# Optimization experiments

Measured on AMD Instinct MI355X. Metric: run time of the kernel, lower is better.

Reference implementation:

```python
import jax, jax.numpy as jnp
import numpy as np
import math

E, H, FFN, NQ = 1024, 16, 4096, 8
B, T = 2, 2048
EPS = 1e-5

def layernorm(x, g, b):
    mu = jnp.mean(x, axis=-1, keepdims=True)
    var = jnp.mean(jnp.square(x - mu), axis=-1, keepdims=True)
    return (x - mu) * jax.lax.rsqrt(var + EPS) * g + b

def setup_inputs() -> dict:
    key = jax.random.key(0)
    ks = jax.random.split(key, 8)
    x = jax.random.normal(ks[0], (B, T, E), dtype=jnp.float32)
    mask = jnp.ones((B, T, T), dtype=bool)
    # constant quantum measurement output: PauliZ expectations of a fixed
    # RandomLayer circuit applied to |0..0> (independent of the input tokens)
    q_out = jax.random.uniform(ks[1], (NQ,), minval=-1.0, maxval=1.0, dtype=jnp.float32)
    s1 = 1.0 / math.sqrt(NQ)
    w1 = jax.random.uniform(ks[2], (NQ, FFN), minval=-s1, maxval=s1, dtype=jnp.float32)
    b1 = jnp.zeros((FFN,), dtype=jnp.float32)
    s2 = 1.0 / math.sqrt(FFN)
    w2 = jax.random.uniform(ks[3], (FFN, E), minval=-s2, maxval=s2, dtype=jnp.float32)
    b2 = jnp.zeros((E,), dtype=jnp.float32)
    g1 = jnp.ones((E,), dtype=jnp.float32); be1 = jnp.zeros((E,), dtype=jnp.float32)
    g2 = jnp.ones((E,), dtype=jnp.float32); be2 = jnp.zeros((E,), dtype=jnp.float32)
    return dict(x=x, mask=mask, q_out=q_out, w1=w1, b1=b1, w2=w2, b2=b2,
                g1=g1, be1=be1, g2=g2, be2=be2)

def reference(x, mask, q_out, w1, b1, w2, b2, g1, be1, g2, be2):
    b, t, e = x.shape
    d_k = e // H
    # q = k = v = head-split x (module has no QKV projections)
    q = x.reshape(b, t, H, d_k).transpose(0, 2, 1, 3)  # [B,H,T,d_k]
    scores = jnp.einsum('bhqd,bhkd->bhqk', q, q) / math.sqrt(d_k)
    scores = jnp.where(mask[:, None, :, :], scores, -1e9)
    attn = jax.nn.softmax(scores, axis=-1)
    out = jnp.einsum('bhqk,bhkd->bhqd', attn, q)
    attn_out = out.transpose(0, 2, 1, 3).reshape(b, t, e)
    x1 = layernorm(x + attn_out, g1, be1)
    # quantum FFN: constant measurement vector broadcast over all tokens
    h = jnp.broadcast_to(q_out, (b, t, NQ))
    h = jnp.dot(h, w1) + b1
    ffn_out = jnp.dot(jax.nn.relu(h), w2) + b2
    return layernorm(x1 + ffn_out, g2, be2)
```

## Files before the change

### kernel.cpp

```cpp
#include <hip/hip_runtime.h>

#define E_   1024
#define H_   16
#define DK_  64
#define FFN_ 4096
#define NQ_  8
#define B_   2
#define T_   2048
#define QBLK 128
#define KVBLK 64
#define NT_  (T_ / KVBLK)

#define NPART 256
#define ROWS_PER_PART (FFN_ / NPART)

typedef __attribute__((ext_vector_type(8))) __bf16 bf16x8;
typedef __attribute__((ext_vector_type(4))) float f32x4;
typedef __attribute__((ext_vector_type(16))) float f32x16;

__device__ __forceinline__ __bf16 tobf(float f) { return (__bf16)f; }

__device__ __forceinline__ unsigned pk2(float a, float b) {
  union { __bf16 h; unsigned short u; } ua, ub;
  ua.h = (__bf16)a; ub.h = (__bf16)b;
  return (unsigned)ua.u | ((unsigned)ub.u << 16);
}

__global__ __launch_bounds__(256)
void cvt_kernel(const float* __restrict__ x, __bf16* __restrict__ xbf,
                __bf16* __restrict__ xbfT) {
  __shared__ __bf16 tile[64][66];
  const int tid = threadIdx.x;
  const int bid = blockIdx.x;
  const int h  = bid & 15;
  const int tt = (bid >> 4) & 31;
  const int b  = bid >> 9;
  const float* src = x + ((size_t)(b * T_ + tt * 64)) * E_ + h * 64;

#pragma unroll
  for (int u = 0; u < 2; ++u) {
    const int idx = tid + 256 * u;
    const int r = idx >> 3;
    const int c = (idx & 7) * 8;
    float4 f0 = *reinterpret_cast<const float4*>(src + (size_t)r * E_ + c);
    float4 f1 = *reinterpret_cast<const float4*>(src + (size_t)r * E_ + c + 4);
    bf16x8 v;
    v[0] = tobf(f0.x); v[1] = tobf(f0.y); v[2] = tobf(f0.z); v[3] = tobf(f0.w);
    v[4] = tobf(f1.x); v[5] = tobf(f1.y); v[6] = tobf(f1.z); v[7] = tobf(f1.w);
    *reinterpret_cast<bf16x8*>(
        &xbf[((size_t)(b * T_ + tt * 64 + r)) * E_ + h * 64 + c]) = v;
#pragma unroll
    for (int j = 0; j < 8; ++j) tile[r][c + j] = v[j];
  }
  __syncthreads();
#pragma unroll
  for (int u = 0; u < 2; ++u) {
    const int idx = tid + 256 * u;
    const int d  = idx >> 3;
    const int tc = (idx & 7) * 8;
    bf16x8 v;
#pragma unroll
    for (int j = 0; j < 8; ++j) v[j] = tile[tc + j][d];
    *reinterpret_cast<bf16x8*>(
        &xbfT[((size_t)((b * H_ + h) * DK_ + d)) * T_ + tt * 64 + tc]) = v;
  }
}

__global__ __launch_bounds__(256)
void ffn_part_kernel(const float* __restrict__ q_out, const float* __restrict__ w1,
                     const float* __restrict__ b1, const float* __restrict__ w2,
                     float* __restrict__ part) {
  __shared__ float h[ROWS_PER_PART];
  const int tid = threadIdx.x;
  const int p = blockIdx.x;
  const int f0 = p * ROWS_PER_PART;
  if (tid < ROWS_PER_PART) {
    const int f = f0 + tid;
    float a = b1[f];
#pragma unroll
    for (int n = 0; n < NQ_; ++n) a += q_out[n] * w1[n * FFN_ + f];
    h[tid] = fmaxf(a, 0.f);
  }
  __syncthreads();
  float4 acc = {0.f, 0.f, 0.f, 0.f};
#pragma unroll
  for (int j = 0; j < ROWS_PER_PART; ++j) {
    const float hf = h[j];
    float4 w = reinterpret_cast<const float4*>(w2 + (size_t)(f0 + j) * E_)[tid];
    acc.x += hf * w.x; acc.y += hf * w.y; acc.z += hf * w.z; acc.w += hf * w.w;
  }
  reinterpret_cast<float4*>(part + (size_t)p * E_)[tid] = acc;
}

__global__ __launch_bounds__(256)
void ffn_reduce_kernel(const float* __restrict__ part, const float* __restrict__ b2,
                       float* __restrict__ ffn_c) {
  const int e = blockIdx.x * 256 + threadIdx.x;
  float a = b2[e];
  for (int r = 0; r < NPART; ++r) a += part[(size_t)r * E_ + e];
  ffn_c[e] = a;
}

#define PV_STEP(KS, DARR, OARR)                                                \
  do {                                                                         \
    const int mA = 2 * ((KS) & 1), mB = mA + 1;                                \
    union { unsigned u[4]; bf16x8 v; } pa;                                     \
    pa.u[0] = hi ? OARR[mB][0] : DARR[mA][0];                                  \
    pa.u[1] = hi ? OARR[mB][1] : DARR[mA][1];                                  \
    pa.u[2] = hi ? DARR[mB][0] : OARR[mA][0];                                  \
    pa.u[3] = hi ? DARR[mB][1] : OARR[mA][1];                                  \
    bf16x8 vb0 = *reinterpret_cast<const bf16x8*>(                             \
        Vtc + rowA + (((32 * (KS) + 16 * hi) ^ rxA)));                         \
    bf16x8 vb1 = *reinterpret_cast<const bf16x8*>(                             \
        Vtc + rowB + (((32 * (KS) + 16 * hi) ^ rxB)));                         \
    acc0 = __builtin_amdgcn_mfma_f32_32x32x16_bf16(pa.v, vb0, acc0, 0, 0, 0);  \
    acc1 = __builtin_amdgcn_mfma_f32_32x32x16_bf16(pa.v, vb1, acc1, 0, 0, 0);  \
  } while (0)

__global__ __launch_bounds__(256)
void attn_kernel(const __bf16* __restrict__ xbf, const __bf16* __restrict__ xbfT,
                 float* __restrict__ out) {
  __shared__ __bf16 Kt[2][KVBLK][DK_ + 8];
  __shared__ __bf16 VtF[2][DK_ * KVBLK];

  const int tid  = threadIdx.x;
  const int wave = tid >> 6;
  const int lane = tid & 63;
  const int l32  = lane & 31;
  const int hi   = lane >> 5;

  const int bh = blockIdx.y;
  const int b  = bh >> 4;
  const int h  = bh & 15;
  const int qbase = blockIdx.x * QBLK;
  const __bf16* xb = xbf + (size_t)b * T_ * E_ + h * DK_;

  bf16x8 qb[4];
  {
    const __bf16 sc = (__bf16)0.125f;
    const __bf16* qrow = xb + (size_t)(qbase + wave * 32 + l32) * E_;
#pragma unroll
    for (int ks = 0; ks < 4; ++ks) {
      bf16x8 v = *reinterpret_cast<const bf16x8*>(qrow + 16 * ks + 8 * hi);
#pragma unroll
      for (int j = 0; j < 8; ++j) v[j] *= sc;
      qb[ks] = v;
    }
  }

  f32x16 acc0, acc1;
#pragma unroll
  for (int j = 0; j < 16; ++j) { acc0[j] = 0.f; acc1[j] = 0.f; }
  float lg = 0.f;

  const int rotA = (l32 & 7) ^ ((l32 >> 3) & 7);
  const int rotB = (l32 & 7) ^ ((4 + (l32 >> 3)) & 7);
  const int rowA = l32 * 128, rxA = rotA << 4;
  const int rowB = (32 + l32) * 128, rxB = rotB << 4;

  const int kp  = tid >> 3;
  const int ds0 = (tid & 7) * 8;
  const __bf16* kbase = xb + (size_t)(2 * kp) * E_ + ds0;
  const int dv = tid >> 3;
  const int kv = (tid & 7) * 8;
  const __bf16* vbase = xbfT + ((size_t)(bh * DK_ + dv)) * T_ + kv;
  const int srotA = (dv & 7) ^ ((dv >> 3) & 7);
  const int dvB = dv + 32;
  const int srotB = (dvB & 7) ^ ((dvB >> 3) & 7);
  const int vbyteA = dv * 128 + ((kv * 2) ^ (srotA << 4));
  const int vbyteB = dvB * 128 + ((kv * 2) ^ (srotB << 4));

  {
    uint4 k0 = *reinterpret_cast<const uint4*>(kbase);
    uint4 k1 = *reinterpret_cast<const uint4*>(kbase + E_);
    uint4 v0 = *reinterpret_cast<const uint4*>(vbase);
    uint4 v1 = *reinterpret_cast<const uint4*>(vbase + (size_t)32 * T_);
    *reinterpret_cast<uint4*>(&Kt[0][2 * kp][ds0])     = k0;
    *reinterpret_cast<uint4*>(&Kt[0][2 * kp + 1][ds0]) = k1;
    char* vb = reinterpret_cast<char*>(&VtF[0][0]);
    *reinterpret_cast<uint4*>(vb + vbyteA) = v0;
    *reinterpret_cast<uint4*>(vb + vbyteB) = v1;
  }
  __syncthreads();

  for (int t = 0; t < NT_; ++t) {
    const int cur = t & 1;
    const __bf16* Ktc = &Kt[cur][0][0];
    const char*   Vtc = reinterpret_cast<const char*>(&VtF[cur][0]);

    uint4 nk0, nk1, nv0, nv1;
    const bool have_next = (t + 1 < NT_);
    if (have_next) {
      const __bf16* nk = kbase + (size_t)(t + 1) * KVBLK * E_;
      const __bf16* nv = vbase + (size_t)(t + 1) * KVBLK;
      nk0 = *reinterpret_cast<const uint4*>(nk);
      nk1 = *reinterpret_cast<const uint4*>(nk + E_);
      nv0 = *reinterpret_cast<const uint4*>(nv);
      nv1 = *reinterpret_cast<const uint4*>(nv + (size_t)32 * T_);
    }

    f32x16 s0, s1;
#pragma unroll
    for (int j = 0; j < 16; ++j) { s0[j] = 0.f; s1[j] = 0.f; }
    __builtin_amdgcn_s_setprio(1);
#pragma unroll
    for (int ks = 0; ks < 4; ++ks) {
      bf16x8 ka0 = *reinterpret_cast<const bf16x8*>(
          Ktc + (size_t)l32 * (DK_ + 8) + 16 * ks + 8 * hi);
      bf16x8 ka1 = *reinterpret_cast<const bf16x8*>(
          Ktc + (size_t)(32 + l32) * (DK_ + 8) + 16 * ks + 8 * hi);
      s0 = __builtin_amdgcn_mfma_f32_32x32x16_bf16(ka0, qb[ks], s0, 0, 0, 0);
      s1 = __builtin_amdgcn_mfma_f32_32x32x16_bf16(ka1, qb[ks], s1, 0, 0, 0);
    }
    __builtin_amdgcn_s_setprio(0);

    unsigned dA_[4][2], dB_[4][2], oA_[4][2], oB_[4][2];
#pragma unroll
    for (int m = 0; m < 4; ++m) {
      float a0 = __expf(s0[4 * m + 0]), a1 = __expf(s0[4 * m + 1]);
      float a2 = __expf(s0[4 * m + 2]), a3 = __expf(s0[4 * m + 3]);
      lg += (a0 + a1) + (a2 + a3);
      dA_[m][0] = pk2(a0, a1); dA_[m][1] = pk2(a2, a3);
      float b0 = __expf(s1[4 * m + 0]), b1 = __expf(s1[4 * m + 1]);
      float b2 = __expf(s1[4 * m + 2]), b3 = __expf(s1[4 * m + 3]);
      lg += (b0 + b1) + (b2 + b3);
      dB_[m][0] = pk2(b0, b1); dB_[m][1] = pk2(b2, b3);
    }
#pragma unroll
    for (int m = 0; m < 4; ++m) {
      oA_[m][0] = (unsigned)__shfl_xor((int)dA_[m][0], 32);
      oA_[m][1] = (unsigned)__shfl_xor((int)dA_[m][1], 32);
      oB_[m][0] = (unsigned)__shfl_xor((int)dB_[m][0], 32);
      oB_[m][1] = (unsigned)__shfl_xor((int)dB_[m][1], 32);
    }

    __builtin_amdgcn_s_setprio(1);
    PV_STEP(0, dA_, oA_);
    PV_STEP(1, dA_, oA_);
    PV_STEP(2, dB_, oB_);
    PV_STEP(3, dB_, oB_);
    __builtin_amdgcn_s_setprio(0);

    if (have_next) {
      const int nxt = cur ^ 1;
      *reinterpret_cast<uint4*>(&Kt[nxt][2 * kp][ds0])     = nk0;
      *reinterpret_cast<uint4*>(&Kt[nxt][2 * kp + 1][ds0]) = nk1;
      char* vb = reinterpret_cast<char*>(&VtF[nxt][0]);
      *reinterpret_cast<uint4*>(vb + vbyteA) = nv0;
      *reinterpret_cast<uint4*>(vb + vbyteB) = nv1;
    }
    __syncthreads();
  }

  lg += __shfl_xor(lg, 32);
#pragma unroll
  for (int r = 0; r < 16; ++r) {
    const int qw = (r & 3) + 8 * (r >> 2) + 4 * hi;
    const float inv = 1.f / __shfl(lg, qw);
    const size_t q = (size_t)b * T_ + qbase + wave * 32 + qw;
    out[q * E_ + h * 64 + l32]      = acc0[r] * inv;
    out[q * E_ + h * 64 + 32 + l32] = acc1[r] * inv;
  }
}

__device__ __forceinline__ float block_sum(float v, float* redrow, int lane, int wave) {
#pragma unroll
  for (int off = 1; off < 64; off <<= 1) v += __shfl_xor(v, off);
  if (lane == 0) redrow[wave] = v;
  __syncthreads();
  return redrow[0] + redrow[1] + redrow[2] + redrow[3];
}

__global__ __launch_bounds__(256)
void ln_kernel(const float* __restrict__ x, const float* __restrict__ ffn_c,
               const float* __restrict__ g1, const float* __restrict__ be1,
               const float* __restrict__ g2, const float* __restrict__ be2,
               float* io) {
  __shared__ float red[4][4];
  const int row = blockIdx.x;
  const int tid = threadIdx.x;
  const int lane = tid & 63, wave = tid >> 6;
  const float* xr = x + (size_t)row * E_;
  float* ior = io + (size_t)row * E_;

  float4 xv = reinterpret_cast<const float4*>(xr)[tid];
  float4 av = reinterpret_cast<const float4*>(ior)[tid];
  float v[4] = {xv.x + av.x, xv.y + av.y, xv.z + av.z, xv.w + av.w};

  float mu1 = block_sum(v[0] + v[1] + v[2] + v[3], red[0], lane, wave) * (1.f / E_);
  float q1 = 0.f;
#pragma unroll
  for (int j = 0; j < 4; ++j) { float d = v[j] - mu1; q1 += d * d; }
  float var1 = block_sum(q1, red[1], lane, wave) * (1.f / E_);
  float rs1 = rsqrtf(var1 + 1e-5f);

  const int e0 = tid * 4;
  float y[4];
#pragma unroll
  for (int j = 0; j < 4; ++j)
    y[j] = (v[j] - mu1) * rs1 * g1[e0 + j] + be1[e0 + j] + ffn_c[e0 + j];

  float mu2 = block_sum(y[0] + y[1] + y[2] + y[3], red[2], lane, wave) * (1.f / E_);
  float q2 = 0.f;
#pragma unroll
  for (int j = 0; j < 4; ++j) { float d = y[j] - mu2; q2 += d * d; }
  float var2 = block_sum(q2, red[3], lane, wave) * (1.f / E_);
  float rs2 = rsqrtf(var2 + 1e-5f);

  float4 o;
  o.x = (y[0] - mu2) * rs2 * g2[e0 + 0] + be2[e0 + 0];
  o.y = (y[1] - mu2) * rs2 * g2[e0 + 1] + be2[e0 + 1];
  o.z = (y[2] - mu2) * rs2 * g2[e0 + 2] + be2[e0 + 2];
  o.w = (y[3] - mu2) * rs2 * g2[e0 + 3] + be2[e0 + 3];
  reinterpret_cast<float4*>(ior)[tid] = o;
}

extern "C" void kernel_launch(void* const* d_in, const int* in_sizes, int n_in,
                              void* d_out, int out_size, void* d_ws, size_t ws_size,
                              hipStream_t stream) {
  (void)in_sizes; (void)n_in; (void)out_size; (void)ws_size;
  const float* x     = (const float*)d_in[0];
  const float* q_out = (const float*)d_in[2];
  const float* w1    = (const float*)d_in[3];
  const float* b1    = (const float*)d_in[4];
  const float* w2    = (const float*)d_in[5];
  const float* b2    = (const float*)d_in[6];
  const float* g1    = (const float*)d_in[7];
  const float* be1   = (const float*)d_in[8];
  const float* g2    = (const float*)d_in[9];
  const float* be2   = (const float*)d_in[10];
  float* out   = (float*)d_out;

  float* ffn_c = (float*)d_ws;
  float* part  = ffn_c + E_;
  __bf16* xbf  = (__bf16*)(part + (size_t)NPART * E_);
  __bf16* xbfT = xbf + (size_t)B_ * T_ * E_;

  cvt_kernel<<<B_ * (T_ / 64) * H_, 256, 0, stream>>>(x, xbf, xbfT);
  ffn_part_kernel<<<NPART, 256, 0, stream>>>(q_out, w1, b1, w2, part);
  ffn_reduce_kernel<<<E_ / 256, 256, 0, stream>>>(part, b2, ffn_c);
  dim3 ag(T_ / QBLK, B_ * H_);
  attn_kernel<<<ag, 256, 0, stream>>>(xbf, xbfT, out);
  ln_kernel<<<B_ * T_, 256, 0, stream>>>(x, ffn_c, g1, be1, g2, be2, out);
}
```

Baseline: 97.10 us.

## Merge prep kernels and streamline attention softmax with exp2 and permlane swap

The bf16 conversion/transpose kernel and the FFN partial kernel become one launch whose block index picks the work, which removes one kernel launch and lets the two jobs overlap. In the attention loop, log2(e) is folded into the query scale so exp2 replaces expf. The cross-half shuffles plus per-lane selects that built the PV operand are replaced by v_permlane32_swap, and bf16 packing now uses a vector conversion. The risks are slightly different bf16 rounding of the pre-scaled query and reliance on an inline-asm instruction specific to the target architecture.

```diff
diff --git a/kernel.cpp b/kernel.cpp
--- a/kernel.cpp
+++ b/kernel.cpp
@@ -13,83 +13,85 @@
 
 #define NPART 256
 #define ROWS_PER_PART (FFN_ / NPART)
+#define CVT_BLOCKS (B_ * (T_ / 64) * H_)
 
 typedef __attribute__((ext_vector_type(8))) __bf16 bf16x8;
+typedef __attribute__((ext_vector_type(2))) __bf16 bf16x2;
+typedef __attribute__((ext_vector_type(2))) float f32x2;
 typedef __attribute__((ext_vector_type(4))) float f32x4;
 typedef __attribute__((ext_vector_type(16))) float f32x16;
 
 __device__ __forceinline__ __bf16 tobf(float f) { return (__bf16)f; }
 
 __device__ __forceinline__ unsigned pk2(float a, float b) {
-  union { __bf16 h; unsigned short u; } ua, ub;
-  ua.h = (__bf16)a; ub.h = (__bf16)b;
-  return (unsigned)ua.u | ((unsigned)ub.u << 16);
+  f32x2 f; f[0] = a; f[1] = b;
+  bf16x2 h = __builtin_convertvector(f, bf16x2);
+  union { bf16x2 h; unsigned u; } u; u.h = h;
+  return u.u;
 }
 
 __global__ __launch_bounds__(256)
-void cvt_kernel(const float* __restrict__ x, __bf16* __restrict__ xbf,
-                __bf16* __restrict__ xbfT) {
-  __shared__ __bf16 tile[64][66];
+void prep_kernel(const float* __restrict__ x, __bf16* __restrict__ xbf,
+                 __bf16* __restrict__ xbfT,
+                 const float* __restrict__ q_out, const float* __restrict__ w1,
+                 const float* __restrict__ b1, const float* __restrict__ w2,
+                 float* __restrict__ part) {
   const int tid = threadIdx.x;
-  const int bid = blockIdx.x;
-  const int h  = bid & 15;
-  const int tt = (bid >> 4) & 31;
-  const int b  = bid >> 9;
-  const float* src = x + ((size_t)(b * T_ + tt * 64)) * E_ + h * 64;
-
-#pragma unroll
-  for (int u = 0; u < 2; ++u) {
-    const int idx = tid + 256 * u;
-    const int r = idx >> 3;
-    const int c = (idx & 7) * 8;
-    float4 f0 = *reinterpret_cast<const float4*>(src + (size_t)r * E_ + c);
-    float4 f1 = *reinterpret_cast<const float4*>(src + (size_t)r * E_ + c + 4);
-    bf16x8 v;
-    v[0] = tobf(f0.x); v[1] = tobf(f0.y); v[2] = tobf(f0.z); v[3] = tobf(f0.w);
-    v[4] = tobf(f1.x); v[5] = tobf(f1.y); v[6] = tobf(f1.z); v[7] = tobf(f1.w);
-    *reinterpret_cast<bf16x8*>(
-        &xbf[((size_t)(b * T_ + tt * 64 + r)) * E_ + h * 64 + c]) = v;
-#pragma unroll
-    for (int j = 0; j < 8; ++j) tile[r][c + j] = v[j];
-  }
-  __syncthreads();
-#pragma unroll
-  for (int u = 0; u < 2; ++u) {
-    const int idx = tid + 256 * u;
-    const int d  = idx >> 3;
-    const int tc = (idx & 7) * 8;
-    bf16x8 v;
-#pragma unroll
-    for (int j = 0; j < 8; ++j) v[j] = tile[tc + j][d];
-    *reinterpret_cast<bf16x8*>(
-        &xbfT[((size_t)((b * H_ + h) * DK_ + d)) * T_ + tt * 64 + tc]) = v;
-  }
-}
-
-__global__ __launch_bounds__(256)
-void ffn_part_kernel(const float* __restrict__ q_out, const float* __restrict__ w1,
-                     const float* __restrict__ b1, const float* __restrict__ w2,
-                     float* __restrict__ part) {
-  __shared__ float h[ROWS_PER_PART];
-  const int tid = threadIdx.x;
-  const int p = blockIdx.x;
-  const int f0 = p * ROWS_PER_PART;
-  if (tid < ROWS_PER_PART) {
-    const int f = f0 + tid;
-    float a = b1[f];
-#pragma unroll
-    for (int n = 0; n < NQ_; ++n) a += q_out[n] * w1[n * FFN_ + f];
-    h[tid] = fmaxf(a, 0.f);
-  }
-  __syncthreads();
-  float4 acc = {0.f, 0.f, 0.f, 0.f};
-#pragma unroll
-  for (int j = 0; j < ROWS_PER_PART; ++j) {
-    const float hf = h[j];
-    float4 w = reinterpret_cast<const float4*>(w2 + (size_t)(f0 + j) * E_)[tid];
-    acc.x += hf * w.x; acc.y += hf * w.y; acc.z += hf * w.z; acc.w += hf * w.w;
-  }
-  reinterpret_cast<float4*>(part + (size_t)p * E_)[tid] = acc;
+  if (blockIdx.x < CVT_BLOCKS) {
+    __shared__ __bf16 tile[64][66];
+    const int bid = blockIdx.x;
+    const int h  = bid & 15;
+    const int tt = (bid >> 4) & 31;
+    const int b  = bid >> 9;
+    const float* src = x + ((size_t)(b * T_ + tt * 64)) * E_ + h * 64;
+#pragma unroll
+    for (int u = 0; u < 2; ++u) {
+      const int idx = tid + 256 * u;
+      const int r = idx >> 3;
+      const int c = (idx & 7) * 8;
+      float4 f0 = *reinterpret_cast<const float4*>(src + (size_t)r * E_ + c);
+      float4 f1 = *reinterpret_cast<const float4*>(src + (size_t)r * E_ + c + 4);
+      bf16x8 v;
+      v[0] = tobf(f0.x); v[1] = tobf(f0.y); v[2] = tobf(f0.z); v[3] = tobf(f0.w);
+      v[4] = tobf(f1.x); v[5] = tobf(f1.y); v[6] = tobf(f1.z); v[7] = tobf(f1.w);
+      *reinterpret_cast<bf16x8*>(
+          &xbf[((size_t)(b * T_ + tt * 64 + r)) * E_ + h * 64 + c]) = v;
+#pragma unroll
+      for (int j = 0; j < 8; ++j) tile[r][c + j] = v[j];
+    }
+    __syncthreads();
+#pragma unroll
+    for (int u = 0; u < 2; ++u) {
+      const int idx = tid + 256 * u;
+      const int d  = idx >> 3;
+      const int tc = (idx & 7) * 8;
+      bf16x8 v;
+#pragma unroll
+      for (int j = 0; j < 8; ++j) v[j] = tile[tc + j][d];
+      *reinterpret_cast<bf16x8*>(
+          &xbfT[((size_t)((b * H_ + h) * DK_ + d)) * T_ + tt * 64 + tc]) = v;
+    }
+  } else {
+    __shared__ float hbuf[ROWS_PER_PART];
+    const int p = blockIdx.x - CVT_BLOCKS;
+    const int f0 = p * ROWS_PER_PART;
+    if (tid < ROWS_PER_PART) {
+      const int f = f0 + tid;
+      float a = b1[f];
+#pragma unroll
+      for (int n = 0; n < NQ_; ++n) a += q_out[n] * w1[n * FFN_ + f];
+      hbuf[tid] = fmaxf(a, 0.f);
+    }
+    __syncthreads();
+    float4 acc = {0.f, 0.f, 0.f, 0.f};
+#pragma unroll
+    for (int j = 0; j < ROWS_PER_PART; ++j) {
+      const float hf = hbuf[j];
+      float4 w = reinterpret_cast<const float4*>(w2 + (size_t)(f0 + j) * E_)[tid];
+      acc.x += hf * w.x; acc.y += hf * w.y; acc.z += hf * w.z; acc.w += hf * w.w;
+    }
+    reinterpret_cast<float4*>(part + (size_t)p * E_)[tid] = acc;
+  }
 }
 
 __global__ __launch_bounds__(256)
@@ -101,20 +103,45 @@
   ffn_c[e] = a;
 }
 
-#define PV_STEP(KS, DARR, OARR)                                                \
+#define SM16(S, P)                                                             \
   do {                                                                         \
-    const int mA = 2 * ((KS) & 1), mB = mA + 1;                                \
+    _Pragma("unroll")                                                          \
+    for (int m = 0; m < 4; ++m) {                                              \
+      float e0 = __builtin_exp2f((S)[4 * m + 0]);                              \
+      float e1 = __builtin_exp2f((S)[4 * m + 1]);                              \
+      float e2 = __builtin_exp2f((S)[4 * m + 2]);                              \
+      float e3 = __builtin_exp2f((S)[4 * m + 3]);                              \
+      lg += (e0 + e1) + (e2 + e3);                                             \
+      (P)[m][0] = pk2(e0, e1); (P)[m][1] = pk2(e2, e3);                        \
+    }                                                                          \
+  } while (0)
+
+#define SWP(a, b) asm volatile("v_permlane32_swap_b32 %0, %1" : "+v"(a), "+v"(b))
+#define SW4(P)                                                                 \
+  do {                                                                         \
+    SWP((P)[0][0], (P)[1][0]); SWP((P)[0][1], (P)[1][1]);                      \
+    SWP((P)[2][0], (P)[3][0]); SWP((P)[2][1], (P)[3][1]);                      \
+  } while (0)
+
+#define PVQ(P, KSG)                                                            \
+  do {                                                                         \
     union { unsigned u[4]; bf16x8 v; } pa;                                     \
-    pa.u[0] = hi ? OARR[mB][0] : DARR[mA][0];                                  \
-    pa.u[1] = hi ? OARR[mB][1] : DARR[mA][1];                                  \
-    pa.u[2] = hi ? DARR[mB][0] : OARR[mA][0];                                  \
-    pa.u[3] = hi ? DARR[mB][1] : OARR[mA][1];                                  \
+    pa.u[0] = (P)[0][0]; pa.u[1] = (P)[0][1];                                  \
+    pa.u[2] = (P)[1][0]; pa.u[3] = (P)[1][1];                                  \
     bf16x8 vb0 = *reinterpret_cast<const bf16x8*>(                             \
-        Vtc + rowA + (((32 * (KS) + 16 * hi) ^ rxA)));                         \
+        Vtc + rowA + ((32 * (KSG) + 16 * hi) ^ rxA));                          \
     bf16x8 vb1 = *reinterpret_cast<const bf16x8*>(                             \
-        Vtc + rowB + (((32 * (KS) + 16 * hi) ^ rxB)));                         \
+        Vtc + rowB + ((32 * (KSG) + 16 * hi) ^ rxB));                          \
     acc0 = __builtin_amdgcn_mfma_f32_32x32x16_bf16(pa.v, vb0, acc0, 0, 0, 0);  \
     acc1 = __builtin_amdgcn_mfma_f32_32x32x16_bf16(pa.v, vb1, acc1, 0, 0, 0);  \
+    pa.u[0] = (P)[2][0]; pa.u[1] = (P)[2][1];                                  \
+    pa.u[2] = (P)[3][0]; pa.u[3] = (P)[3][1];                                  \
+    bf16x8 vc0 = *reinterpret_cast<const bf16x8*>(                             \
+        Vtc + rowA + ((32 * ((KSG) + 1) + 16 * hi) ^ rxA));                    \
+    bf16x8 vc1 = *reinterpret_cast<const bf16x8*>(                             \
+        Vtc + rowB + ((32 * ((KSG) + 1) + 16 * hi) ^ rxB));                    \
+    acc0 = __builtin_amdgcn_mfma_f32_32x32x16_bf16(pa.v, vc0, acc0, 0, 0, 0);  \
+    acc1 = __builtin_amdgcn_mfma_f32_32x32x16_bf16(pa.v, vc1, acc1, 0, 0, 0);  \
   } while (0)
 
 __global__ __launch_bounds__(256)
@@ -137,13 +164,13 @@
 
   bf16x8 qb[4];
   {
-    const __bf16 sc = (__bf16)0.125f;
+    const float sc = 0.125f * 1.44269504088896f;
     const __bf16* qrow = xb + (size_t)(qbase + wave * 32 + l32) * E_;
 #pragma unroll
     for (int ks = 0; ks < 4; ++ks) {
       bf16x8 v = *reinterpret_cast<const bf16x8*>(qrow + 16 * ks + 8 * hi);
 #pragma unroll
-      for (int j = 0; j < 8; ++j) v[j] *= sc;
+      for (int j = 0; j < 8; ++j) v[j] = tobf((float)v[j] * sc);
       qb[ks] = v;
     }
   }
@@ -153,10 +180,11 @@
   for (int j = 0; j < 16; ++j) { acc0[j] = 0.f; acc1[j] = 0.f; }
   float lg = 0.f;
 
-  const int rotA = (l32 & 7) ^ ((l32 >> 3) & 7);
-  const int rotB = (l32 & 7) ^ ((4 + (l32 >> 3)) & 7);
-  const int rowA = l32 * 128, rxA = rotA << 4;
-  const int rowB = (32 + l32) * 128, rxB = rotB << 4;
+  const int rowA = l32 * 128;
+  const int rxA  = ((l32 & 7) ^ ((l32 >> 3) & 7)) << 4;
+  const int d2   = 32 + l32;
+  const int rowB = d2 * 128;
+  const int rxB  = ((d2 & 7) ^ ((d2 >> 3) & 7)) << 4;
 
   const int kp  = tid >> 3;
   const int ds0 = (tid & 7) * 8;
@@ -164,11 +192,11 @@
   const int dv = tid >> 3;
   const int kv = (tid & 7) * 8;
   const __bf16* vbase = xbfT + ((size_t)(bh * DK_ + dv)) * T_ + kv;
-  const int srotA = (dv & 7) ^ ((dv >> 3) & 7);
-  const int dvB = dv + 32;
-  const int srotB = (dvB & 7) ^ ((dvB >> 3) & 7);
-  const int vbyteA = dv * 128 + ((kv * 2) ^ (srotA << 4));
-  const int vbyteB = dvB * 128 + ((kv * 2) ^ (srotB << 4));
+  const int srA = ((dv & 7) ^ ((dv >> 3) & 7)) << 4;
+  const int dv2 = dv + 32;
+  const int srB = ((dv2 & 7) ^ ((dv2 >> 3) & 7)) << 4;
+  const int vbyteA = dv * 128 + ((kv * 2) ^ srA);
+  const int vbyteB = dv2 * 128 + ((kv * 2) ^ srB);
 
   {
     uint4 k0 = *reinterpret_cast<const uint4*>(kbase);
@@ -214,31 +242,15 @@
     }
     __builtin_amdgcn_s_setprio(0);
 
-    unsigned dA_[4][2], dB_[4][2], oA_[4][2], oB_[4][2];
-#pragma unroll
-    for (int m = 0; m < 4; ++m) {
-      float a0 = __expf(s0[4 * m + 0]), a1 = __expf(s0[4 * m + 1]);
-      float a2 = __expf(s0[4 * m + 2]), a3 = __expf(s0[4 * m + 3]);
-      lg += (a0 + a1) + (a2 + a3);
-      dA_[m][0] = pk2(a0, a1); dA_[m][1] = pk2(a2, a3);
-      float b0 = __expf(s1[4 * m + 0]), b1 = __expf(s1[4 * m + 1]);
-      float b2 = __expf(s1[4 * m + 2]), b3 = __expf(s1[4 * m + 3]);
-      lg += (b0 + b1) + (b2 + b3);
-      dB_[m][0] = pk2(b0, b1); dB_[m][1] = pk2(b2, b3);
-    }
-#pragma unroll
-    for (int m = 0; m < 4; ++m) {
-      oA_[m][0] = (unsigned)__shfl_xor((int)dA_[m][0], 32);
-      oA_[m][1] = (unsigned)__shfl_xor((int)dA_[m][1], 32);
-      oB_[m][0] = (unsigned)__shfl_xor((int)dB_[m][0], 32);
-      oB_[m][1] = (unsigned)__shfl_xor((int)dB_[m][1], 32);
-    }
+    unsigned dA_[4][2], dB_[4][2];
+    SM16(s0, dA_);
+    SM16(s1, dB_);
+    SW4(dA_);
+    SW4(dB_);
 
     __builtin_amdgcn_s_setprio(1);
-    PV_STEP(0, dA_, oA_);
-    PV_STEP(1, dA_, oA_);
-    PV_STEP(2, dB_, oB_);
-    PV_STEP(3, dB_, oB_);
+    PVQ(dA_, 0);
+    PVQ(dB_, 2);
     __builtin_amdgcn_s_setprio(0);
 
     if (have_next) {
@@ -336,8 +348,8 @@
   __bf16* xbf  = (__bf16*)(part + (size_t)NPART * E_);
   __bf16* xbfT = xbf + (size_t)B_ * T_ * E_;
 
-  cvt_kernel<<<B_ * (T_ / 64) * H_, 256, 0, stream>>>(x, xbf, xbfT);
-  ffn_part_kernel<<<NPART, 256, 0, stream>>>(q_out, w1, b1, w2, part);
+  prep_kernel<<<CVT_BLOCKS + NPART, 256, 0, stream>>>(x, xbf, xbfT, q_out, w1,
+                                                      b1, w2, part);
   ffn_reduce_kernel<<<E_ / 256, 256, 0, stream>>>(part, b2, ffn_c);
   dim3 ag(T_ / QBLK, B_ * H_);
   attn_kernel<<<ag, 256, 0, stream>>>(xbf, xbfT, out);
```

Result: no change. 97.63 us (+0.5%).
